# Performance work log

Measured on AMD Instinct MI355X. Metric: run time of the kernel, lower is better.

## Reference

```python
import jax, jax.numpy as jnp
import numpy as np

HIDDEN = 2048
NH = 32        # query heads
NKV = 4        # kv heads
D = 128        # head dim
T = 2048       # tokens
WINDOW = 512   # sliding window
EPS = 1e-6
THETA = 1000000.0
SCALE = D ** -0.5


def setup_inputs() -> dict:
    key = jax.random.key(0)
    k1, k2, k3 = jax.random.split(key, 3)
    return {
        "positions": jnp.arange(T, dtype=jnp.int64) if jax.config.jax_enable_x64 else jnp.arange(T, dtype=jnp.int32),
        "hidden_states": jax.random.normal(k1, (T, HIDDEN), dtype=jnp.float32),
        "w_qkv": jax.random.normal(k2, (HIDDEN, (NH + 2 * NKV) * D), dtype=jnp.float32) * 0.02,
        "w_o": jax.random.normal(k3, (NH * D, HIDDEN), dtype=jnp.float32) * 0.02,
        "q_norm_w": jnp.ones((D,), dtype=jnp.float32),
        "k_norm_w": jnp.ones((D,), dtype=jnp.float32),
    }


def _rms_norm(x, w):
    # x: [..., D]; per-head RMSNorm
    var = jnp.mean(x * x, axis=-1, keepdims=True)
    return x * jax.lax.rsqrt(var + EPS) * w


def _rope(x, positions):
    # x: [T, H, D], neox-style rotary over full head dim
    inv_freq = 1.0 / (THETA ** (jnp.arange(0, D, 2, dtype=jnp.float32) / D))  # [D/2]
    freqs = positions.astype(jnp.float32)[:, None] * inv_freq                 # [T, D/2]
    cos = jnp.cos(freqs)[:, None, :]
    sin = jnp.sin(freqs)[:, None, :]
    x1, x2 = x[..., : D // 2], x[..., D // 2 :]
    return jnp.concatenate([x1 * cos - x2 * sin, x2 * cos + x1 * sin], axis=-1)


def reference(positions, hidden_states, w_qkv, w_o, q_norm_w, k_norm_w):
    qkv = hidden_states @ w_qkv                                   # [T, (NH+2NKV)*D]
    q, k, v = jnp.split(qkv, [NH * D, (NH + NKV) * D], axis=-1)
    q = _rms_norm(q.reshape(T, NH, D), q_norm_w)
    k = _rms_norm(k.reshape(T, NKV, D), k_norm_w)
    v = v.reshape(T, NKV, D)
    q = _rope(q, positions)
    k = _rope(k, positions)
    # GQA: expand kv heads to query heads
    rep = NH // NKV
    k = jnp.repeat(k, rep, axis=1)                                # [T, NH, D]
    v = jnp.repeat(v, rep, axis=1)
    scores = jnp.einsum("qhd,khd->hqk", q, k) * SCALE             # [NH, T, T]
    i = jnp.arange(T)[:, None]
    j = jnp.arange(T)[None, :]
    mask = (j <= i) & (i - j < WINDOW)                            # causal sliding window
    scores = jnp.where(mask[None, :, :], scores, jnp.finfo(scores.dtype).min)
    probs = jax.nn.softmax(scores, axis=-1)
    out = jnp.einsum("hqk,khd->qhd", probs, v).reshape(T, NH * D)
    return out @ w_o
```

## Files before the change

### kernel.cpp

```cpp
#include <hip/hip_runtime.h>
#include <math.h>

#define T      2048
#define HIDDEN 2048
#define NH     32
#define NKV    4
#define D      128
#define WINDOW 512
#define QKVW   ((NH + 2 * NKV) * D)
#define ODIM   (NH * D)
#define EPS    1e-6f
#define SCALE  0.08838834764831845f
#define PSTR   68
#define ESTR   136
#define VSTR   36
#define QMUL   ((float)(0.08838834764831845 * 1.4426950408889634))
#define MLOG2E 5.7707801635558536f

typedef _Float16 f16x8 __attribute__((ext_vector_type(8)));
typedef _Float16 f16x4 __attribute__((ext_vector_type(4)));
typedef float    f32x4 __attribute__((ext_vector_type(4)));


__device__ __forceinline__ void gl2lds16(const void* g, void* l) {
  __builtin_amdgcn_global_load_lds((const __attribute__((address_space(1))) void*)g,
                                   (__attribute__((address_space(3))) void*)l,
                                   16, 0, 0);
}

#define NB_A  2048
#define NB_B1 5120
#define NB_B2 4096
__global__ __launch_bounds__(256)
void prep(const float* __restrict__ hidden, const float* __restrict__ w_qkv,
          const float* __restrict__ w_o, const int* __restrict__ positions,
          _Float16* __restrict__ Ah1, _Float16* __restrict__ Bp1,
          _Float16* __restrict__ Bp2, float* __restrict__ cosT,
          float* __restrict__ sinT) {
  const int bx = blockIdx.x;
  const int tid = threadIdx.x;
  if (bx < NB_A) {
    const int cid = bx * 256 + tid;
    const int c = cid & 63;
    const int tile = cid >> 6;
    const int mtg = tile & (T / 16 - 1);
    const int kt = tile >> 7;
    const float* src = hidden + (size_t)(mtg * 16 + (c & 15)) * HIDDEN + kt * 32 + (c >> 4) * 8;
    const float4 a = *(const float4*)src;
    const float4 b = *(const float4*)(src + 4);
    f16x8 h;
    h[0] = (_Float16)a.x; h[1] = (_Float16)a.y; h[2] = (_Float16)a.z; h[3] = (_Float16)a.w;
    h[4] = (_Float16)b.x; h[5] = (_Float16)b.y; h[6] = (_Float16)b.z; h[7] = (_Float16)b.w;
    *(f16x8*)(Ah1 + (size_t)cid * 8) = h;
  } else if (bx < NB_A + NB_B1) {
    const int cid = (bx - NB_A) * 256 + tid;
    const int c = cid & 63;
    const int tile = cid >> 6;
    const int ntg = tile % (QKVW >> 4);
    const int kt = tile / (QKVW >> 4);
    const float* src = w_qkv + (size_t)(kt * 32 + (c >> 4) * 8) * QKVW + ntg * 16 + (c & 15);
    f16x8 h;
#pragma unroll
    for (int j = 0; j < 8; ++j) h[j] = (_Float16)src[(size_t)j * QKVW];
    *(f16x8*)(Bp1 + (size_t)cid * 8) = h;
  } else if (bx < NB_A + NB_B1 + NB_B2) {
    const int cid = (bx - NB_A - NB_B1) * 256 + tid;
    const int c = cid & 63;
    const int tile = cid >> 6;
    const int ntg = tile & (HIDDEN / 16 - 1);
    const int kt = tile >> 7;
    const float* src = w_o + (size_t)(kt * 32 + (c >> 4) * 8) * HIDDEN + ntg * 16 + (c & 15);
    f16x8 h;
#pragma unroll
    for (int j = 0; j < 8; ++j) h[j] = (_Float16)src[(size_t)j * HIDDEN];
    *(f16x8*)(Bp2 + (size_t)cid * 8) = h;
  } else {
    const int p0 = (bx - NB_A - NB_B1 - NB_B2) * 64 + (tid >> 6) * 16;
    const int j = tid & 63;
    const float invf = (float)pow(1.0e6, -(double)j / 64.0);
#pragma unroll 4
    for (int i = 0; i < 16; ++i) {
      const int t = p0 + i;
      const float ang = (float)positions[t] * invf;
      cosT[t * 64 + j] = cosf(ang);
      sinT[t * 64 + j] = sinf(ang);
    }
  }
}

#define KSTEPS 64

__global__ __launch_bounds__(256, 3)
void gemm_qkv(const _Float16* __restrict__ Apk, const _Float16* __restrict__ Bpk,
              const float* __restrict__ qnw, const float* __restrict__ knw,
              const float* __restrict__ cosT, const float* __restrict__ sinT,
              _Float16* __restrict__ Qpk, _Float16* __restrict__ Kpk,
              _Float16* __restrict__ Vpk) {
  extern __shared__ _Float16 SM[];
  const int tid = threadIdx.x;
  const int lane = tid & 63;
  const int wv = tid >> 6;
  const int l15 = lane & 15;
  const int l4 = lane >> 4;
  const int bx = blockIdx.x, by = blockIdx.y;

  f32x4 acc[2][8];
#pragma unroll
  for (int i = 0; i < 2; ++i)
#pragma unroll
    for (int j = 0; j < 8; ++j) acc[i][j] = (f32x4)0.f;

  auto stage = [&](int k, int s) {
    const int u = wv * 4 + s;
    char* dst = (char*)SM + (k % 3) * 16384 +
                (u < 8 ? u * 1024 : 8192 + (u - 8) * 1024);
    const char* src = (u < 8)
        ? (const char*)Apk + ((size_t)k * (T / 16) + by * 8 + u) * 1024 + lane * 16
        : (const char*)Bpk + ((size_t)k * (QKVW / 16) + bx * 8 + (u - 8)) * 1024 + lane * 16;
    gl2lds16(src, dst);
  };

#pragma unroll
  for (int k = 0; k < 2; ++k)
#pragma unroll
    for (int s = 0; s < 4; ++s) stage(k, s);
  asm volatile("s_waitcnt vmcnt(4)" ::: "memory");
  __builtin_amdgcn_s_barrier();
  __builtin_amdgcn_sched_barrier(0);

  int slot = 0;
  for (int t = 0; t < KSTEPS; ++t) {
    const _Float16* As = SM + slot * 8192;
    const _Float16* Bs = As + 4096;
    f16x8 af[2], bf[8];
#pragma unroll
    for (int i = 0; i < 2; ++i)
      af[i] = *(const f16x8*)(As + (wv * 2 + i) * 512 + lane * 8);
#pragma unroll
    for (int j = 0; j < 8; ++j)
      bf[j] = *(const f16x8*)(Bs + j * 512 + lane * 8);
    if (t + 2 < KSTEPS)
#pragma unroll
      for (int s = 0; s < 4; ++s) stage(t + 2, s);
    __builtin_amdgcn_s_setprio(1);
#pragma unroll
    for (int i = 0; i < 2; ++i)
#pragma unroll
      for (int j = 0; j < 8; ++j)
        acc[i][j] = __builtin_amdgcn_mfma_f32_16x16x32_f16(af[i], bf[j], acc[i][j], 0, 0, 0);
    __builtin_amdgcn_s_setprio(0);
    if (t < KSTEPS - 2)       asm volatile("s_waitcnt vmcnt(4)" ::: "memory");
    else if (t == KSTEPS - 2) asm volatile("s_waitcnt vmcnt(0)" ::: "memory");
    __builtin_amdgcn_s_barrier();
    __builtin_amdgcn_sched_barrier(0);
    slot = (slot == 2) ? 0 : slot + 1;
  }
  __syncthreads();

  if (bx < NH + NKV) {
    const bool isq = bx < NH;
    const float* w = isq ? qnw : knw;
    const float omul = isq ? QMUL : 1.0f;
    float wcol[8];
#pragma unroll
    for (int j = 0; j < 8; ++j) wcol[j] = w[j * 16 + l15];

    _Float16* ex = SM + wv * (32 * ESTR);
#pragma unroll
    for (int i = 0; i < 2; ++i)
#pragma unroll
      for (int r = 0; r < 4; ++r) {
        float ss = 0.f;
#pragma unroll
        for (int j = 0; j < 8; ++j) ss += acc[i][j][r] * acc[i][j][r];
        ss += __shfl_xor(ss, 1); ss += __shfl_xor(ss, 2);
        ss += __shfl_xor(ss, 4); ss += __shfl_xor(ss, 8);
        const float rn = 1.0f / sqrtf(ss * (1.0f / D) + EPS);
        const int row = i * 16 + l4 * 4 + r;
        const int t = by * 128 + wv * 32 + row;
#pragma unroll
        for (int j = 0; j < 4; ++j) {
          const int jc = j * 16 + l15;
          const float c = cosT[t * 64 + jc];
          const float s = sinT[t * 64 + jc];
          const float x1 = acc[i][j][r] * rn * wcol[j];
          const float x2 = acc[i][j + 4][r] * rn * wcol[j + 4];
          ex[row * ESTR + jc]      = (_Float16)((x1 * c - x2 * s) * omul);
          ex[row * ESTR + 64 + jc] = (_Float16)((x2 * c + x1 * s) * omul);
        }
      }
    const int hl = isq ? bx : bx - NH;
    _Float16* dst0 = isq ? Qpk : Kpk;
#pragma unroll
    for (int u = 0; u < 2; ++u) {
      const int qt = by * 8 + wv * 2 + u;
#pragma unroll
      for (int ds = 0; ds < 4; ++ds) {
        const f16x8 frag = *(const f16x8*)(ex + (u * 16 + l15) * ESTR + ds * 32 + l4 * 8);
        *(f16x8*)(dst0 + ((size_t)(hl * 128 + qt) * 4 + ds) * 512 + lane * 8) = frag;
      }
    }
  } else {
    const int kvh = bx - NH - NKV;
    _Float16* exv = SM + wv * (128 * VSTR);
#pragma unroll
    for (int i = 0; i < 2; ++i)
#pragma unroll
      for (int j = 0; j < 8; ++j) {
        f16x4 v4;
#pragma unroll
        for (int r = 0; r < 4; ++r) v4[r] = (_Float16)acc[i][j][r];
        *(f16x4*)(exv + (j * 16 + l15) * VSTR + i * 16 + l4 * 4) = v4;
      }
    const int kt64 = by * 2 + (wv >> 1);
    const int ks = wv & 1;
#pragma unroll
    for (int dt = 0; dt < 8; ++dt) {
      const f16x4 lo = *(const f16x4*)(exv + (dt * 16 + l15) * VSTR + l4 * 8);
      const f16x4 hi = *(const f16x4*)(exv + (dt * 16 + l15) * VSTR + l4 * 8 + 4);
      f16x8 h8;
#pragma unroll
      for (int r = 0; r < 4; ++r) { h8[r] = lo[r]; h8[r + 4] = hi[r]; }
      *(f16x8*)(Vpk + (((size_t)(kvh * 32 + kt64) * 2 + ks) * 8 + dt) * 512 + lane * 8) = h8;
    }
  }
}

__global__ __launch_bounds__(256, 3)
void gemm_f16p(const _Float16* __restrict__ Apk, const _Float16* __restrict__ Bpk,
               float* __restrict__ C0, float* __restrict__ C1,
               int M, int N, int nkt) {
  extern __shared__ _Float16 SM[];
  const int tid = threadIdx.x;
  const int lane = tid & 63;
  const int wv = tid >> 6;
  const int wr = wv & 1, wc = wv >> 1;
  const int kt0 = blockIdx.z * nkt;
  float* __restrict__ C = blockIdx.z ? C1 : C0;

  f32x4 acc[4][4];
#pragma unroll
  for (int i = 0; i < 4; ++i)
#pragma unroll
    for (int j = 0; j < 4; ++j) acc[i][j] = (f32x4)0.f;

  const size_t Astep = (size_t)(M >> 4) * 1024;
  const size_t Bstep = (size_t)(N >> 4) * 1024;
  const char* Ag = (const char*)Apk + (size_t)kt0 * Astep +
                   (size_t)(blockIdx.y * 8) * 1024 + lane * 16;
  const char* Bg = (const char*)Bpk + (size_t)kt0 * Bstep +
                   (size_t)(blockIdx.x * 8) * 1024 + lane * 16;

  auto stage = [&](int k, int s) {
    const int u = wv * 4 + s;
    char* dst = (char*)SM + (k % 3) * 16384 +
                (u < 8 ? u * 1024 : 8192 + (u - 8) * 1024);
    const char* src = (u < 8) ? Ag + (size_t)k * Astep + u * 1024
                              : Bg + (size_t)k * Bstep + (u - 8) * 1024;
    gl2lds16(src, dst);
  };

#pragma unroll
  for (int k = 0; k < 2; ++k)
#pragma unroll
    for (int s = 0; s < 4; ++s) stage(k, s);
  asm volatile("s_waitcnt vmcnt(4)" ::: "memory");
  __builtin_amdgcn_s_barrier();
  __builtin_amdgcn_sched_barrier(0);

  int slot = 0;
  for (int t = 0; t < nkt; ++t) {
    const _Float16* As = SM + slot * 8192;
    const _Float16* Bs = As + 4096;
    f16x8 af[4], bf[4];
#pragma unroll
    for (int i = 0; i < 4; ++i)
      af[i] = *(const f16x8*)(As + (wr * 4 + i) * 512 + lane * 8);
#pragma unroll
    for (int j = 0; j < 4; ++j)
      bf[j] = *(const f16x8*)(Bs + (wc * 4 + j) * 512 + lane * 8);
    if (t + 2 < nkt)
#pragma unroll
      for (int s = 0; s < 4; ++s) stage(t + 2, s);
    __builtin_amdgcn_s_setprio(1);
#pragma unroll
    for (int i = 0; i < 4; ++i)
#pragma unroll
      for (int j = 0; j < 4; ++j)
        acc[i][j] = __builtin_amdgcn_mfma_f32_16x16x32_f16(af[i], bf[j], acc[i][j], 0, 0, 0);
    __builtin_amdgcn_s_setprio(0);
    if (t < nkt - 2)       asm volatile("s_waitcnt vmcnt(4)" ::: "memory");
    else if (t == nkt - 2) asm volatile("s_waitcnt vmcnt(0)" ::: "memory");
    __builtin_amdgcn_s_barrier();
    __builtin_amdgcn_sched_barrier(0);
    slot = (slot == 2) ? 0 : slot + 1;
  }

  const int row0 = blockIdx.y * 128 + wr * 64 + ((lane >> 4) << 2);
  const int col0 = blockIdx.x * 128 + wc * 64 + (lane & 15);
#pragma unroll
  for (int i = 0; i < 4; ++i)
#pragma unroll
    for (int j = 0; j < 4; ++j) {
#pragma unroll
      for (int r = 0; r < 4; ++r)
        C[(size_t)(row0 + i * 16 + r) * N + col0 + j * 16] = acc[i][j][r];
    }
}

__global__ __launch_bounds__(256)
void reduce_add(const float4* __restrict__ a, const float4* __restrict__ b,
                float4* __restrict__ o, int n4) {
  for (int i = blockIdx.x * 256 + threadIdx.x; i < n4; i += gridDim.x * 256) {
    const float4 x = a[i], y = b[i];
    o[i] = make_float4(x.x + y.x, x.y + y.y, x.z + y.z, x.w + y.w);
  }
}

__global__ __launch_bounds__(256)
void attn_mfma(const _Float16* __restrict__ Qpk, const _Float16* __restrict__ Kpk,
               const _Float16* __restrict__ Vpk, _Float16* __restrict__ Ap2) {
  const int h = blockIdx.x;
  const int q0 = blockIdx.y * 128;
  const int kvh = h >> 3;
  const int tid = threadIdx.x;
  const int lane = tid & 63;
  const int wv = tid >> 6;
  const int l15 = lane & 15;
  const int l4 = lane >> 4;

  __shared__ _Float16 SM[8192 + 8192 + 4 * 32 * PSTR];
  _Float16* Ks = SM;
  _Float16* Vs = SM + 8192;
  _Float16* Pw = SM + 16384 + wv * 32 * PSTR;

  f16x8 qfA[4], qfB[4];
  {
    const _Float16* qa = Qpk + ((size_t)h * 128 + (q0 >> 4) + wv * 2) * 2048 + lane * 8;
#pragma unroll
    for (int ds = 0; ds < 4; ++ds) {
      qfA[ds] = *(const f16x8*)(qa + ds * 512);
      qfB[ds] = *(const f16x8*)(qa + 2048 + ds * 512);
    }
  }

  f16x8 ones;
#pragma unroll
  for (int j = 0; j < 8; ++j) ones[j] = (_Float16)1.0f;

  f32x4 OA[8], OB[8];
#pragma unroll
  for (int dt = 0; dt < 8; ++dt) { OA[dt] = (f32x4)0.f; OB[dt] = (f32x4)0.f; }
  f32x4 LA = (f32x4)0.f, LB = (f32x4)0.f;

  int kstart = q0 - (WINDOW - 1);
  if (kstart < 0) kstart = 0;
  kstart &= ~63;

  for (int kt = kstart; kt < q0 + 128; kt += 64) {
    __syncthreads();
    const _Float16* Kg = Kpk + ((size_t)kvh * 128 + (kt >> 4)) * 2048 + lane * 8;
    const _Float16* Vg = Vpk + ((size_t)kvh * 32 + (kt >> 6)) * 8192 + lane * 8;
#pragma unroll
    for (int t = wv; t < 16; t += 4) {
      gl2lds16(Kg + t * 512, (char*)Ks + t * 1024);
      gl2lds16(Vg + t * 512, (char*)Vs + t * 1024);
    }
    __syncthreads();

    f32x4 sA[4], sB[4];
#pragma unroll
    for (int nt = 0; nt < 4; ++nt) { sA[nt] = (f32x4)(-MLOG2E); sB[nt] = (f32x4)(-MLOG2E); }
    __builtin_amdgcn_s_setprio(1);
#pragma unroll
    for (int ds = 0; ds < 4; ++ds) {
#pragma unroll
      for (int nt = 0; nt < 4; ++nt) {
        const f16x8 kf = *(const f16x8*)(Ks + (nt * 4 + ds) * 512 + lane * 8);
        sA[nt] = __builtin_amdgcn_mfma_f32_16x16x32_f16(qfA[ds], kf, sA[nt], 0, 0, 0);
        sB[nt] = __builtin_amdgcn_mfma_f32_16x16x32_f16(qfB[ds], kf, sB[nt], 0, 0, 0);
      }
    }
    __builtin_amdgcn_s_setprio(0);

    const int qbA = q0 + wv * 32 + l4 * 4;
    const int kb = kt + l15;
#pragma unroll
    for (int nt = 0; nt < 4; ++nt) {
      const int kidx = kb + nt * 16;
#pragma unroll
      for (int r = 0; r < 4; ++r) {
        float pA = __builtin_amdgcn_exp2f(sA[nt][r]);
        float pB = __builtin_amdgcn_exp2f(sB[nt][r]);
        pA = ((unsigned)(qbA + r - kidx) < WINDOW) ? pA : 0.f;
        pB = ((unsigned)(qbA + 16 + r - kidx) < WINDOW) ? pB : 0.f;
        Pw[(l4 * 4 + r) * PSTR + nt * 16 + l15] = (_Float16)pA;
        Pw[(16 + l4 * 4 + r) * PSTR + nt * 16 + l15] = (_Float16)pB;
      }
    }

    __builtin_amdgcn_s_setprio(1);
#pragma unroll
    for (int ks = 0; ks < 2; ++ks) {
      const f16x8 pfA = *(const f16x8*)(Pw + l15 * PSTR + ks * 32 + l4 * 8);
      const f16x8 pfB = *(const f16x8*)(Pw + (16 + l15) * PSTR + ks * 32 + l4 * 8);
      LA = __builtin_amdgcn_mfma_f32_16x16x32_f16(pfA, ones, LA, 0, 0, 0);
      LB = __builtin_amdgcn_mfma_f32_16x16x32_f16(pfB, ones, LB, 0, 0, 0);
#pragma unroll
      for (int dt = 0; dt < 8; ++dt) {
        const f16x8 vf = *(const f16x8*)(Vs + (ks * 8 + dt) * 512 + lane * 8);
        OA[dt] = __builtin_amdgcn_mfma_f32_16x16x32_f16(pfA, vf, OA[dt], 0, 0, 0);
        OB[dt] = __builtin_amdgcn_mfma_f32_16x16x32_f16(pfB, vf, OB[dt], 0, 0, 0);
      }
    }
    __builtin_amdgcn_s_setprio(0);
  }

  __syncthreads();
  _Float16* Tw = SM + wv * 16 * ESTR;
#pragma unroll
  for (int half = 0; half < 2; ++half) {
    const f32x4* O = half ? OB : OA;
    const f32x4  L = half ? LB : LA;
    float inv[4];
#pragma unroll
    for (int r = 0; r < 4; ++r) inv[r] = 1.0f / L[r];
#pragma unroll
    for (int dt = 0; dt < 8; ++dt)
#pragma unroll
      for (int r = 0; r < 4; ++r)
        Tw[(l4 * 4 + r) * ESTR + dt * 16 + l15] = (_Float16)(O[dt][r] * inv[r]);
    const int qt = (q0 >> 4) + wv * 2 + half;
#pragma unroll
    for (int ds = 0; ds < 4; ++ds) {
      const f16x8 frag = *(const f16x8*)(Tw + l15 * ESTR + ds * 32 + l4 * 8);
      *(f16x8*)(Ap2 + ((size_t)(h * 4 + ds) * 128 + qt) * 512 + lane * 8) = frag;
    }
  }
}

extern "C" void kernel_launch(void* const* d_in, const int* in_sizes, int n_in,
                              void* d_out, int out_size, void* d_ws, size_t ws_size,
                              hipStream_t stream) {
  const int*   positions = (const int*)d_in[0];
  const float* hidden    = (const float*)d_in[1];
  const float* w_qkv     = (const float*)d_in[2];
  const float* w_o       = (const float*)d_in[3];
  const float* q_norm_w  = (const float*)d_in[4];
  const float* k_norm_w  = (const float*)d_in[5];
  float* out = (float*)d_out;

  char* ws = (char*)d_ws;
  _Float16* Kpk = (_Float16*)ws;
  _Float16* Vpk = Kpk + (size_t)T * NKV * D;
  ws += (size_t)T * QKVW * 4;
  _Float16* Ap2 = (_Float16*)ws;
  float* P0 = (float*)(ws + (size_t)T * ODIM * 2);
  ws += (size_t)T * ODIM * 4;
  float* cosT = (float*)ws;  ws += (size_t)T * 64 * 4;
  float* sinT = (float*)ws;  ws += (size_t)T * 64 * 4;
  _Float16* Bp1 = (_Float16*)ws; ws += (size_t)HIDDEN * QKVW * 2;
  _Float16* Bp2 = (_Float16*)ws; ws += (size_t)ODIM * HIDDEN * 2;
  _Float16* Ah1 = (_Float16*)ws; ws += (size_t)T * HIDDEN * 2;
  _Float16* Qpk = (_Float16*)ws;
  float* P1 = (float*)Qpk;
  ws += (size_t)T * ODIM * 2;

  prep<<<dim3(NB_A + NB_B1 + NB_B2 + T / 64), 256, 0, stream>>>(
      hidden, w_qkv, w_o, positions, Ah1, Bp1, Bp2, cosT, sinT);

  gemm_qkv<<<dim3(QKVW / 128, T / 128), 256, 49152, stream>>>(
      Ah1, Bp1, q_norm_w, k_norm_w, cosT, sinT, Qpk, Kpk, Vpk);

  attn_mfma<<<dim3(NH, T / 128), 256, 0, stream>>>(Qpk, Kpk, Vpk, Ap2);

  gemm_f16p<<<dim3(HIDDEN / 128, T / 128, 2), 256, 49152, stream>>>(
      Ap2, Bp2, P0, P1, T, HIDDEN, ODIM / 32 / 2);
  reduce_add<<<dim3(1024), 256, 0, stream>>>((const float4*)P0, (const float4*)P1,
                                             (float4*)out, T * HIDDEN / 4);
}
```

Measured before the change: 276.3 us.

## Prefetch next K/V tile during softmax and PV in attention loop

Restructures the attention inner loop so the next tile's K and V loads into shared memory are issued right after the QK^T MFMAs finish. The softmax and PV matmul for the current tile then run while those loads are in flight. K is overwritten in place (safe after a barrier) and V is double-buffered, which adds 16KB of LDS per block. The cost is higher LDS use, which may reduce occupancy, plus manual waitcnt/barrier synchronisation that must stay correct.

Result: no change. 279.3 us (+1.1%).

```diff
diff --git a/kernel.cpp b/kernel.cpp
--- a/kernel.cpp
+++ b/kernel.cpp
@@ -329,10 +329,10 @@
   const int l15 = lane & 15;
   const int l4 = lane >> 4;
 
-  __shared__ _Float16 SM[8192 + 8192 + 4 * 32 * PSTR];
+  __shared__ _Float16 SM[8192 + 2 * 8192 + 4 * 32 * PSTR];
   _Float16* Ks = SM;
   _Float16* Vs = SM + 8192;
-  _Float16* Pw = SM + 16384 + wv * 32 * PSTR;
+  _Float16* Pw = SM + 24576 + wv * 32 * PSTR;
 
   f16x8 qfA[4], qfB[4];
   {
@@ -356,18 +356,25 @@
   int kstart = q0 - (WINDOW - 1);
   if (kstart < 0) kstart = 0;
   kstart &= ~63;
-
-  for (int kt = kstart; kt < q0 + 128; kt += 64) {
-    __syncthreads();
-    const _Float16* Kg = Kpk + ((size_t)kvh * 128 + (kt >> 4)) * 2048 + lane * 8;
-    const _Float16* Vg = Vpk + ((size_t)kvh * 32 + (kt >> 6)) * 8192 + lane * 8;
+  const int kend = q0 + 128;
+
+  auto stageKV = [&](int kt2, int vb) {
+    const _Float16* Kg = Kpk + ((size_t)kvh * 128 + (kt2 >> 4)) * 2048 + lane * 8;
+    const _Float16* Vg = Vpk + ((size_t)kvh * 32 + (kt2 >> 6)) * 8192 + lane * 8;
 #pragma unroll
     for (int t = wv; t < 16; t += 4) {
       gl2lds16(Kg + t * 512, (char*)Ks + t * 1024);
-      gl2lds16(Vg + t * 512, (char*)Vs + t * 1024);
-    }
-    __syncthreads();
-
+      gl2lds16(Vg + t * 512, (char*)(Vs + vb * 8192) + t * 1024);
+    }
+  };
+
+  stageKV(kstart, 0);
+  asm volatile("s_waitcnt vmcnt(0)" ::: "memory");
+  __builtin_amdgcn_s_barrier();
+  __builtin_amdgcn_sched_barrier(0);
+
+  int vbuf = 0;
+  for (int kt = kstart; kt < kend; kt += 64) {
     f32x4 sA[4], sB[4];
 #pragma unroll
     for (int nt = 0; nt < 4; ++nt) { sA[nt] = (f32x4)(-MLOG2E); sB[nt] = (f32x4)(-MLOG2E); }
@@ -382,6 +389,9 @@
       }
     }
     __builtin_amdgcn_s_setprio(0);
+    __builtin_amdgcn_s_barrier();
+    __builtin_amdgcn_sched_barrier(0);
+    if (kt + 64 < kend) stageKV(kt + 64, vbuf ^ 1);
 
     const int qbA = q0 + wv * 32 + l4 * 4;
     const int kb = kt + l15;
@@ -399,6 +409,7 @@
       }
     }
 
+    const _Float16* Vcur = Vs + vbuf * 8192;
     __builtin_amdgcn_s_setprio(1);
 #pragma unroll
     for (int ks = 0; ks < 2; ++ks) {
@@ -408,15 +419,18 @@
       LB = __builtin_amdgcn_mfma_f32_16x16x32_f16(pfB, ones, LB, 0, 0, 0);
 #pragma unroll
       for (int dt = 0; dt < 8; ++dt) {
-        const f16x8 vf = *(const f16x8*)(Vs + (ks * 8 + dt) * 512 + lane * 8);
+        const f16x8 vf = *(const f16x8*)(Vcur + (ks * 8 + dt) * 512 + lane * 8);
         OA[dt] = __builtin_amdgcn_mfma_f32_16x16x32_f16(pfA, vf, OA[dt], 0, 0, 0);
         OB[dt] = __builtin_amdgcn_mfma_f32_16x16x32_f16(pfB, vf, OB[dt], 0, 0, 0);
       }
     }
     __builtin_amdgcn_s_setprio(0);
-  }
-
-  __syncthreads();
+    asm volatile("s_waitcnt vmcnt(0)" ::: "memory");
+    __builtin_amdgcn_s_barrier();
+    __builtin_amdgcn_sched_barrier(0);
+    vbuf ^= 1;
+  }
+
   _Float16* Tw = SM + wv * 16 * ESTR;
 #pragma unroll
   for (int half = 0; half < 2; ++half) {
```
